# Kernel optimization log

Hardware: AMD Instinct MI355X
Metric: run time of the kernel (lower is better)

Reference implementation:

```python
import jax, jax.numpy as jnp
from jax import lax
import numpy as np


def _conv3x3(x, w, b):
    # x: [B,C,H,W], w: [O,I,3,3] (OIHW), SAME padding, stride 1
    y = lax.conv_general_dilated(x, w, window_strides=(1, 1), padding='SAME',
                                 dimension_numbers=('NCHW', 'OIHW', 'NCHW'))
    return y + b[None, :, None, None]


def setup_inputs() -> dict:
    key = jax.random.key(0)
    ks = jax.random.split(key, 9)
    B, C, H, W = 4, 64, 64, 64
    wscale = 1.0 / np.sqrt(C * 9)  # keep conv outputs / attention logits sane
    x = jax.random.normal(ks[0], (B, C, H, W), dtype=jnp.float32)
    wq = jax.random.normal(ks[1], (C, C, 3, 3), dtype=jnp.float32) * wscale
    bq = jax.random.normal(ks[2], (C,), dtype=jnp.float32) * 0.1
    wk = jax.random.normal(ks[3], (C, C, 3, 3), dtype=jnp.float32) * wscale
    bk = jax.random.normal(ks[4], (C,), dtype=jnp.float32) * 0.1
    wv = jax.random.normal(ks[5], (C, C, 3, 3), dtype=jnp.float32) * wscale
    bv = jax.random.normal(ks[6], (C,), dtype=jnp.float32) * 0.1
    pos_gamma = jax.random.normal(ks[7], (1,), dtype=jnp.float32)
    chan_gamma = jax.random.normal(ks[8], (1,), dtype=jnp.float32)
    return {'x': x, 'wq': wq, 'bq': bq, 'wk': wk, 'bk': bk, 'wv': wv, 'bv': bv,
            'pos_gamma': pos_gamma, 'chan_gamma': chan_gamma}


def reference(x, wq, bq, wk, bk, wv, bv, pos_gamma, chan_gamma):
    B, C, H, W = x.shape
    N = H * W
    # position (spatial) self-attention over N = H*W locations
    q = _conv3x3(x, wq, bq).reshape(B, C, N)
    k = _conv3x3(x, wk, bk).reshape(B, C, N)
    v = _conv3x3(x, wv, bv).reshape(B, C, N)
    # attn[b,i,j] = softmax_j( sum_c q[b,c,i] * k[b,c,j] )
    pos_attn = jax.nn.softmax(jnp.einsum('bci,bcj->bij', q, k), axis=-1)
    # pos_out[b,c,j] = sum_i v[b,c,i] * attn[b,i,j]  (matches torch.bmm(v, attn))
    pos = jnp.einsum('bci,bij->bcj', v, pos_attn).reshape(B, C, H, W)
    pos_out = pos_gamma * pos + x
    # channel self-attention over C channels (x is its own q/k/v)
    xf = x.reshape(B, C, N)
    chan_attn = jax.nn.softmax(jnp.einsum('bcn,bdn->bcd', xf, xf), axis=-1)
    chan = jnp.einsum('bcd,bdn->bcn', chan_attn, xf).reshape(B, C, H, W)
    chan_out = chan_gamma * chan + x
    return pos_out + chan_out
```

## Files before the change

### kernel.cpp

```cpp
#include <hip/hip_runtime.h>

#define OFF_Q2    1048576u
#define OFF_K2    2097152u
#define OFF_V2    3145728u
#define OFF_X2    3670016u
#define OFF_WT    4194304u
#define OFF_INVL  4452352u
#define OFF_A     4730880u
#define WS_FLOATS 4747264u

typedef short s8v __attribute__((ext_vector_type(8)));
typedef float f16v __attribute__((ext_vector_type(16)));

#define MFMA32(a, b, c) __builtin_amdgcn_mfma_f32_32x32x16_bf16((a), (b), (c), 0, 0, 0)

__device__ __forceinline__ unsigned short bf16_rne(float f) {
    union { float f; unsigned int u; } v; v.f = f;
    unsigned int r = v.u + 0x7FFFu + ((v.u >> 16) & 1u);
    return (unsigned short)(r >> 16);
}
__device__ __forceinline__ float bf2f(unsigned short h) {
    union { unsigned int u; float f; } t; t.u = ((unsigned int)h) << 16;
    return t.f;
}
__device__ __forceinline__ void split2(float f, unsigned short& h, unsigned short& l) {
    unsigned short hh = bf16_rne(f);
    h = hh;
    l = bf16_rne(f - bf2f(hh));
}
__device__ __forceinline__ unsigned int cvtpk(float lo, float hi) {
    unsigned int r;
    asm("v_cvt_pk_bf16_f32 %0, %1, %2" : "=v"(r) : "v"(lo), "v"(hi));
    return r;
}
__device__ __forceinline__ void pl32swap(unsigned int& a, unsigned int& b) {
    asm volatile("v_permlane32_swap_b32 %0, %1" : "+v"(a), "+v"(b));
}
__device__ __forceinline__ s8v mk8(unsigned int w0, unsigned int w1,
                                   unsigned int w2, unsigned int w3) {
    union { unsigned int u[4]; s8v v; } t;
    t.u[0] = w0; t.u[1] = w1; t.u[2] = w2; t.u[3] = w3;
    return t.v;
}
__device__ __forceinline__ f16v zero16() {
    f16v z;
#pragma unroll
    for (int i = 0; i < 16; ++i) z[i] = 0.0f;
    return z;
}


__global__ void k_wtrans(const float* __restrict__ wq, const float* __restrict__ wk,
                         const float* __restrict__ wv, unsigned short* __restrict__ wf) {
    int t = blockIdx.x * 256 + threadIdx.x;
    int f = t >> 9, pos = t & 511;
    int lane = pos >> 3, e = pos & 7;
    int oc = f & 1, kst = (f >> 1) & 3;
    int ct = f >> 3;
    int tap = ct % 9, conv = ct / 9;
    int o = oc * 32 + (lane & 31);
    int ci = kst * 16 + (lane >> 5) * 8 + e;
    const float* w = (conv == 0) ? wq : (conv == 1) ? wk : wv;
    float v = w[(o * 64 + ci) * 9 + tap];
    unsigned short hh, ll;
    split2(v, hh, ll);
    wf[(f * 2 + 0) * 512 + pos] = hh;
    wf[(f * 2 + 1) * 512 + pos] = ll;
}

__global__ __launch_bounds__(256) void k_xpack(const float* __restrict__ x,
                                               unsigned short* __restrict__ X2,
                                               unsigned short* __restrict__ XV2) {
    int gid = blockIdx.x * 256 + threadIdx.x;
    int b = gid >> 16;
    int c = (gid >> 10) & 63;
    int n4 = (gid & 1023) * 4;
    float4 v = *(const float4*)(x + (size_t)(b * 64 + c) * 4096 + n4);
    unsigned short hv[4] = {bf16_rne(v.x), bf16_rne(v.y), bf16_rne(v.z), bf16_rne(v.w)};
    int kst = c >> 4, e = c & 7, hb = (c >> 3) & 1;
#pragma unroll
    for (int u = 0; u < 4; ++u) {
        int n = n4 + u;
        int nch = n >> 5, lane = (n & 31) + 32 * hb;
        X2[(size_t)((b * 128 + nch) * 4 + kst) * 512 + lane * 8 + e] = hv[u];
    }
    int ich = n4 >> 5, ksub = (n4 >> 4) & 1, cb = c >> 5;
    int lane2 = (c & 31) + 32 * ((n4 >> 3) & 1);
    size_t xi = (size_t)(((b * 128 + ich) * 2 + ksub) * 2 + cb) * 512 + lane2 * 8 + (n4 & 7);
    unsigned long long w = (unsigned long long)hv[0]
                         | ((unsigned long long)hv[1] << 16)
                         | ((unsigned long long)hv[2] << 32)
                         | ((unsigned long long)hv[3] << 48);
    *(unsigned long long*)(XV2 + xi) = w;
}

__global__ __launch_bounds__(384) void k_conv(
        const float* __restrict__ x, const unsigned short* __restrict__ wf,
        const float* __restrict__ bq, const float* __restrict__ bk, const float* __restrict__ bv,
        unsigned short* __restrict__ Q2, unsigned short* __restrict__ K2,
        unsigned short* __restrict__ V2) {
    int nb = blockIdx.x;
    int b = blockIdx.y;
    int h = nb >> 1, w0 = (nb & 1) * 32;

    __shared__ unsigned short xwh[6528];
    __shared__ unsigned short xwl[6528];

    int tid = threadIdx.x;
    for (int idx = tid; idx < 6528; idx += 384) {
        int W = idx % 34;
        int c = (idx / 34) & 63;
        int dy = idx / (34 * 64);
        int hs = h + dy - 1, wi = w0 + W - 1;
        float v = 0.0f;
        if (hs >= 0 && hs < 64 && wi >= 0 && wi < 64)
            v = x[((b * 64 + c) * 64 + hs) * 64 + wi];
        unsigned short hh_, ll_;
        split2(v, hh_, ll_);
        int row = dy * 34 + W;
        int byt = row * 128 + c * 2;
        int swz = byt ^ ((row & 7) << 4);
        *(unsigned short*)((char*)xwh + swz) = hh_;
        *(unsigned short*)((char*)xwl + swz) = ll_;
    }
    __syncthreads();

    int lane = tid & 63, wv = tid >> 6;
    int conv = wv >> 1, oc = wv & 1;
    int hh = lane >> 5, l31 = lane & 31;

    const float* bias = (conv == 0) ? bq : (conv == 1) ? bk : bv;
    f16v D;
    if (conv < 2) {
#pragma unroll
        for (int r = 0; r < 16; ++r)
            D[r] = bias[oc * 32 + (r & 3) + 8 * (r >> 2) + 4 * hh];
    } else {
        float bvv = bias[oc * 32 + l31];
#pragma unroll
        for (int r = 0; r < 16; ++r) D[r] = bvv;
    }

#pragma unroll
    for (int tap = 0; tap < 9; ++tap) {
        int dy = tap / 3, dx = tap % 3;
#pragma unroll
        for (int kst = 0; kst < 4; ++kst) {
            int f = ((conv * 9 + tap) * 4 + kst) * 2 + oc;
            s8v Wh = *(const s8v*)(wf + (f * 2 + 0) * 512 + lane * 8);
            s8v Wl = *(const s8v*)(wf + (f * 2 + 1) * 512 + lane * 8);
            int row = dy * 34 + dx + l31;
            int byt = row * 128 + kst * 32 + hh * 16;
            int swz = byt ^ ((row & 7) << 4);
            s8v Xh = *(const s8v*)((const char*)xwh + swz);
            s8v Xl = *(const s8v*)((const char*)xwl + swz);
            if (conv < 2) {
                D = MFMA32(Wh, Xh, D);
                D = MFMA32(Wh, Xl, D);
                D = MFMA32(Wl, Xh, D);
            } else {
                D = MFMA32(Xh, Wh, D);
                D = MFMA32(Xl, Wh, D);
                D = MFMA32(Xh, Wl, D);
            }
        }
    }

    if (conv < 2) {
        unsigned short sh[16], sl[16];
#pragma unroll
        for (int r = 0; r < 16; ++r) split2(D[r], sh[r], sl[r]);
        unsigned int ah0 = sh[0] | ((unsigned int)sh[1] << 16), ah1 = sh[2] | ((unsigned int)sh[3] << 16);
        unsigned int ah2 = sh[4] | ((unsigned int)sh[5] << 16), ah3 = sh[6] | ((unsigned int)sh[7] << 16);
        pl32swap(ah0, ah2); pl32swap(ah1, ah3);
        s8v F0h = mk8(ah0, ah1, ah2, ah3);
        unsigned int al0 = sl[0] | ((unsigned int)sl[1] << 16), al1 = sl[2] | ((unsigned int)sl[3] << 16);
        unsigned int al2 = sl[4] | ((unsigned int)sl[5] << 16), al3 = sl[6] | ((unsigned int)sl[7] << 16);
        pl32swap(al0, al2); pl32swap(al1, al3);
        s8v F0l = mk8(al0, al1, al2, al3);
        unsigned int bh0 = sh[8] | ((unsigned int)sh[9] << 16), bh1 = sh[10] | ((unsigned int)sh[11] << 16);
        unsigned int bh2 = sh[12] | ((unsigned int)sh[13] << 16), bh3 = sh[14] | ((unsigned int)sh[15] << 16);
        pl32swap(bh0, bh2); pl32swap(bh1, bh3);
        s8v F1h = mk8(bh0, bh1, bh2, bh3);
        unsigned int bl0 = sl[8] | ((unsigned int)sl[9] << 16), bl1 = sl[10] | ((unsigned int)sl[11] << 16);
        unsigned int bl2 = sl[12] | ((unsigned int)sl[13] << 16), bl3 = sl[14] | ((unsigned int)sl[15] << 16);
        pl32swap(bl0, bl2); pl32swap(bl1, bl3);
        s8v F1l = mk8(bl0, bl1, bl2, bl3);
        unsigned short* dst = (conv == 0) ? Q2 : K2;
        size_t b0 = (size_t)(((b * 128 + nb) * 4 + oc * 2 + 0) * 2) * 512 + lane * 8;
        size_t b1 = (size_t)(((b * 128 + nb) * 4 + oc * 2 + 1) * 2) * 512 + lane * 8;
        *(s8v*)(dst + b0) = F0h;
        *(s8v*)(dst + b0 + 512) = F0l;
        *(s8v*)(dst + b1) = F1h;
        *(s8v*)(dst + b1 + 512) = F1l;
    } else {
        unsigned int a0 = cvtpk(D[0], D[1]),  a1 = cvtpk(D[2], D[3]);
        unsigned int a2 = cvtpk(D[4], D[5]),  a3 = cvtpk(D[6], D[7]);
        pl32swap(a0, a2); pl32swap(a1, a3);
        s8v F0h = mk8(a0, a1, a2, a3);
        unsigned int b0w = cvtpk(D[8], D[9]),  b1w = cvtpk(D[10], D[11]);
        unsigned int b2w = cvtpk(D[12], D[13]), b3w = cvtpk(D[14], D[15]);
        pl32swap(b0w, b2w); pl32swap(b1w, b3w);
        s8v F1h = mk8(b0w, b1w, b2w, b3w);
        size_t v0 = (size_t)(((b * 128 + nb) * 2 + 0) * 2 + oc) * 512 + lane * 8;
        size_t v1 = (size_t)(((b * 128 + nb) * 2 + 1) * 2 + oc) * 512 + lane * 8;
        *(s8v*)(V2 + v0) = F0h;
        *(s8v*)(V2 + v1) = F1h;
    }
}

__global__ __launch_bounds__(256) void k_gram(const unsigned short* __restrict__ XV2,
                                              float* __restrict__ Gp) {
    int kp = blockIdx.x, b = blockIdx.y;
    int tid = threadIdx.x, lane = tid & 63, wv = tid >> 6;
    int cb1 = wv & 1, cb2 = wv >> 1;
    f16v G = zero16();
#pragma unroll 1
    for (int t = 0; t < 32; ++t) {
        int ich = kp * 32 + t;
        const unsigned short* base = XV2 + (size_t)(b * 128 + ich) * 2048 + lane * 8;
        s8v a0 = *(const s8v*)(base + (0 * 2 + cb1) * 512);
        s8v b0 = *(const s8v*)(base + (0 * 2 + cb2) * 512);
        s8v a1 = *(const s8v*)(base + (1 * 2 + cb1) * 512);
        s8v b1 = *(const s8v*)(base + (1 * 2 + cb2) * 512);
        G = MFMA32(a0, b0, G);
        G = MFMA32(a1, b1, G);
    }
    int hh = lane >> 5, l31 = lane & 31;
#pragma unroll
    for (int r = 0; r < 16; ++r) {
        int cc = cb1 * 32 + (r & 3) + 8 * (r >> 2) + 4 * hh;
        int dd = cb2 * 32 + l31;
        Gp[(size_t)(kp * 4 + b) * 4096 + cc * 64 + dd] = G[r];
    }
}

__global__ void k_asm(const float* __restrict__ Gp, unsigned short* __restrict__ A2) {
    int row = blockIdx.x;
    int d = threadIdx.x;
    int b = row >> 6, c = row & 63;
    float g = 0.0f;
#pragma unroll
    for (int p = 0; p < 4; ++p) g += Gp[(size_t)(p * 4 + b) * 4096 + c * 64 + d];
    float mx = g;
    for (int off = 32; off >= 1; off >>= 1) mx = fmaxf(mx, __shfl_xor(mx, off, 64));
    float e = __expf(g - mx);
    float s = e;
    for (int off = 32; off >= 1; off >>= 1) s += __shfl_xor(s, off, 64);
    float a = e / s;
    int cb = c >> 5, kst = d >> 4;
    int lane2 = (c & 31) + 32 * ((d >> 3) & 1);
    A2[(size_t)((b * 2 + cb) * 4 + kst) * 512 + lane2 * 8 + (d & 7)] = bf16_rne(a);
}

__global__ __launch_bounds__(512) void k_pass1(
        const unsigned short* __restrict__ Q2, const unsigned short* __restrict__ K2,
        float* __restrict__ invl) {
    int flat = blockIdx.x;
    int xcd = flat & 7;
    int b = xcd >> 1;
    int ich = (xcd & 1) * 64 + (flat >> 3);
    int tid = threadIdx.x, lane = tid & 63, wv = tid >> 6;

    __shared__ float lsum[8][32];

    const unsigned short* qp = Q2 + (size_t)(b * 128 + ich) * 4096 + lane * 8;
    s8v qf0 = *(const s8v*)(qp);
    s8v qf1 = *(const s8v*)(qp + 512);
    s8v qf2 = *(const s8v*)(qp + 1024);
    s8v qf3 = *(const s8v*)(qp + 1536);
    s8v qf4 = *(const s8v*)(qp + 2048);
    s8v qf5 = *(const s8v*)(qp + 2560);
    s8v qf6 = *(const s8v*)(qp + 3072);
    s8v qf7 = *(const s8v*)(qp + 3584);

    float la0 = 0.f, la1 = 0.f;
#pragma unroll 1
    for (int t = 0; t < 16; ++t) {
        int jch = wv * 16 + t;
        const unsigned short* kp = K2 + (size_t)(b * 128 + jch) * 4096 + lane * 8;
        s8v kf0 = *(const s8v*)(kp);
        s8v kf1 = *(const s8v*)(kp + 512);
        s8v kf2 = *(const s8v*)(kp + 1024);
        s8v kf3 = *(const s8v*)(kp + 1536);
        s8v kf4 = *(const s8v*)(kp + 2048);
        s8v kf5 = *(const s8v*)(kp + 2560);
        s8v kf6 = *(const s8v*)(kp + 3072);
        s8v kf7 = *(const s8v*)(kp + 3584);
        f16v Sa = zero16(), Sb = zero16();
        Sa = MFMA32(kf0, qf0, Sa);
        Sa = MFMA32(kf0, qf1, Sa);
        Sa = MFMA32(kf1, qf0, Sa);
        Sa = MFMA32(kf2, qf2, Sa);
        Sa = MFMA32(kf2, qf3, Sa);
        Sa = MFMA32(kf3, qf2, Sa);
        Sb = MFMA32(kf4, qf4, Sb);
        Sb = MFMA32(kf4, qf5, Sb);
        Sb = MFMA32(kf5, qf4, Sb);
        Sb = MFMA32(kf6, qf6, Sb);
        Sb = MFMA32(kf6, qf7, Sb);
        Sb = MFMA32(kf7, qf6, Sb);
#pragma unroll
        for (int r = 0; r < 8; ++r) la0 += __expf(Sa[r] + Sb[r]);
#pragma unroll
        for (int r = 8; r < 16; ++r) la1 += __expf(Sa[r] + Sb[r]);
    }
    float lacc = la0 + la1;
    lacc += __shfl_xor(lacc, 32);
    if (lane < 32) lsum[wv][lane] = lacc;
    __syncthreads();
    if (tid < 32) {
        float s = 0.f;
#pragma unroll
        for (int p = 0; p < 8; ++p) s += lsum[p][tid];
        invl[b * 4096 + ich * 32 + tid] = 1.0f / s;
    }
}

__global__ __launch_bounds__(256) void k_vnorm(
        unsigned short* __restrict__ V2, const float* __restrict__ invl) {
    int u = blockIdx.x * 256 + threadIdx.x;
    int lane = u & 63, ksub = (u >> 7) & 1;
    int ich = (u >> 8) & 127, b = u >> 15;
    int n0 = ich * 32 + ksub * 16 + (lane >> 5) * 8;
    size_t base = (size_t)u * 8;
    s8v vh = *(s8v*)(V2 + base);
    float4 iv0 = *(const float4*)(invl + b * 4096 + n0);
    float4 iv1 = *(const float4*)(invl + b * 4096 + n0 + 4);
    float ivv[8] = {iv0.x, iv0.y, iv0.z, iv0.w, iv1.x, iv1.y, iv1.z, iv1.w};
    s8v o;
#pragma unroll
    for (int e = 0; e < 8; ++e)
        o[e] = (short)bf16_rne(bf2f((unsigned short)vh[e]) * ivv[e]);
    *(s8v*)(V2 + base) = o;
}

__global__ __launch_bounds__(512) void k_pass2(
        const unsigned short* __restrict__ Q2, const unsigned short* __restrict__ K2,
        const unsigned short* __restrict__ V2, const unsigned short* __restrict__ X2,
        const unsigned short* __restrict__ A2, const float* __restrict__ x,
        const float* __restrict__ pg, const float* __restrict__ cg,
        float* __restrict__ out) {
    int flat = blockIdx.x;
    int xcd = flat & 7;
    int b = xcd >> 1;
    int jt = (xcd & 1) * 64 + (flat >> 3);
    int tid = threadIdx.x, lane = tid & 63, wv = tid >> 6;

    __shared__ float rlds[8][64][32];

    const unsigned short* kp = K2 + (size_t)(b * 128 + jt) * 4096 + lane * 8;
    s8v kf0 = *(const s8v*)(kp);
    s8v kf1 = *(const s8v*)(kp + 512);
    s8v kf2 = *(const s8v*)(kp + 1024);
    s8v kf3 = *(const s8v*)(kp + 1536);
    s8v kf4 = *(const s8v*)(kp + 2048);
    s8v kf5 = *(const s8v*)(kp + 2560);
    s8v kf6 = *(const s8v*)(kp + 3072);
    s8v kf7 = *(const s8v*)(kp + 3584);

    f16v O0 = zero16(), O1 = zero16();

#pragma unroll 1
    for (int t = 0; t < 16; ++t) {
        int ich = wv * 16 + t;
        const unsigned short* qp = Q2 + (size_t)(b * 128 + ich) * 4096 + lane * 8;
        s8v qf0 = *(const s8v*)(qp);
        s8v qf1 = *(const s8v*)(qp + 512);
        s8v qf2 = *(const s8v*)(qp + 1024);
        s8v qf3 = *(const s8v*)(qp + 1536);
        s8v qf4 = *(const s8v*)(qp + 2048);
        s8v qf5 = *(const s8v*)(qp + 2560);
        s8v qf6 = *(const s8v*)(qp + 3072);
        s8v qf7 = *(const s8v*)(qp + 3584);
        const unsigned short* vp = V2 + (size_t)(b * 128 + ich) * 2048 + lane * 8;
        s8v vA = *(const s8v*)(vp);
        s8v vB = *(const s8v*)(vp + 512);
        s8v vC = *(const s8v*)(vp + 1024);
        s8v vD = *(const s8v*)(vp + 1536);

        f16v Sa = zero16(), Sb = zero16();
        Sa = MFMA32(qf0, kf0, Sa);
        Sa = MFMA32(qf0, kf1, Sa);
        Sa = MFMA32(qf1, kf0, Sa);
        Sa = MFMA32(qf2, kf2, Sa);
        Sa = MFMA32(qf2, kf3, Sa);
        Sa = MFMA32(qf3, kf2, Sa);
        Sb = MFMA32(qf4, kf4, Sb);
        Sb = MFMA32(qf4, kf5, Sb);
        Sb = MFMA32(qf5, kf4, Sb);
        Sb = MFMA32(qf6, kf6, Sb);
        Sb = MFMA32(qf6, kf7, Sb);
        Sb = MFMA32(qf7, kf6, Sb);

        float p[16];
#pragma unroll
        for (int r = 0; r < 16; ++r) p[r] = __expf(Sa[r] + Sb[r]);

        unsigned int a0 = cvtpk(p[0], p[1]),  a1 = cvtpk(p[2], p[3]);
        unsigned int a2 = cvtpk(p[4], p[5]),  a3 = cvtpk(p[6], p[7]);
        pl32swap(a0, a2);
        pl32swap(a1, a3);
        s8v P0 = mk8(a0, a1, a2, a3);
        unsigned int b0 = cvtpk(p[8], p[9]),  b1 = cvtpk(p[10], p[11]);
        unsigned int b2 = cvtpk(p[12], p[13]), b3 = cvtpk(p[14], p[15]);
        pl32swap(b0, b2);
        pl32swap(b1, b3);
        s8v P1 = mk8(b0, b1, b2, b3);

        O0 = MFMA32(vA, P0, O0);
        O0 = MFMA32(vC, P1, O0);
        O1 = MFMA32(vB, P0, O1);
        O1 = MFMA32(vD, P1, O1);
    }

    int hh = lane >> 5, jj = lane & 31;
#pragma unroll
    for (int r = 0; r < 16; ++r) {
        int c = (r & 3) + 8 * (r >> 2) + 4 * hh;
        rlds[wv][c][jj] = O0[r];
        rlds[wv][c + 32][jj] = O1[r];
    }
    __syncthreads();
    float sums[4];
#pragma unroll
    for (int k = 0; k < 4; ++k) {
        int el = tid + k * 512;
        int c = el >> 5, j2 = el & 31;
        float s = 0.f;
#pragma unroll
        for (int p = 0; p < 8; ++p) s += rlds[p][c][j2];
        sums[k] = s;
    }
    __syncthreads();
    float* sb = &rlds[0][0][0];
    if (wv < 2) {
        int cb = wv;
        f16v Dc = zero16();
#pragma unroll
        for (int kst = 0; kst < 4; ++kst) {
            s8v af = *(const s8v*)(A2 + (size_t)((b * 2 + cb) * 4 + kst) * 512 + lane * 8);
            s8v xf = *(const s8v*)(X2 + (size_t)((b * 128 + jt) * 4 + kst) * 512 + lane * 8);
            Dc = MFMA32(af, xf, Dc);
        }
#pragma unroll
        for (int r = 0; r < 16; ++r) {
            int c = cb * 32 + (r & 3) + 8 * (r >> 2) + 4 * hh;
            sb[c * 33 + jj] = Dc[r];
        }
    }
#pragma unroll
    for (int k = 0; k < 4; ++k) {
        int el = tid + k * 512;
        int c = el >> 5, j2 = el & 31;
        sb[2112 + el] = x[(size_t)(b * 64 + c) * 4096 + jt * 32 + j2];
    }
    __syncthreads();
    float pgv = pg[0], cgv = cg[0];
#pragma unroll
    for (int k = 0; k < 4; ++k) {
        int el = tid + k * 512;
        int c = el >> 5, j2 = el & 31;
        out[(size_t)(b * 64 + c) * 4096 + jt * 32 + j2] =
            pgv * sums[k] + cgv * sb[c * 33 + j2] + 2.0f * sb[2112 + el];
    }
}

extern "C" void kernel_launch(void* const* d_in, const int* in_sizes, int n_in,
                              void* d_out, int out_size, void* d_ws, size_t ws_size,
                              hipStream_t stream) {
    const float* x  = (const float*)d_in[0];
    const float* wq = (const float*)d_in[1];
    const float* bq = (const float*)d_in[2];
    const float* wk = (const float*)d_in[3];
    const float* bk = (const float*)d_in[4];
    const float* wv = (const float*)d_in[5];
    const float* bv = (const float*)d_in[6];
    const float* pg = (const float*)d_in[7];
    const float* cg = (const float*)d_in[8];
    float* out = (float*)d_out;

    if (ws_size < (size_t)WS_FLOATS * sizeof(float)) return;
    float* ws = (float*)d_ws;
    float* Gp = ws;
    unsigned short* XV2 = (unsigned short*)(ws + 65536);
    unsigned short* Q2  = (unsigned short*)(ws + OFF_Q2);
    unsigned short* K2  = (unsigned short*)(ws + OFF_K2);
    unsigned short* V2  = (unsigned short*)(ws + OFF_V2);
    unsigned short* X2  = (unsigned short*)(ws + OFF_X2);
    unsigned short* wfb = (unsigned short*)(ws + OFF_WT);
    float* invl = ws + OFF_INVL;
    unsigned short* A2  = (unsigned short*)(ws + OFF_A);

    k_wtrans<<<432, 256, 0, stream>>>(wq, wk, wv, wfb);
    k_xpack<<<1024, 256, 0, stream>>>(x, X2, XV2);
    k_conv<<<dim3(128, 4), 384, 0, stream>>>(x, wfb, bq, bk, bv, Q2, K2, V2);
    k_gram<<<dim3(4, 4), 256, 0, stream>>>(XV2, Gp);
    k_asm<<<256, 64, 0, stream>>>(Gp, A2);
    k_pass1<<<512, 512, 0, stream>>>(Q2, K2, invl);
    k_vnorm<<<512, 256, 0, stream>>>(V2, invl);
    k_pass2<<<512, 512, 0, stream>>>(Q2, K2, V2, X2, A2, x, pg, cg, out);
}
```

Measured before the change: 124.8 us.

## Split gram over more blocks, double pass1 waves, halve pass2 reduction LDS

The Gram kernel is split into 16 partial blocks per batch instead of 4, with a fully unrolled 8-step loop, and the assemble kernel sums 16 partials. Gp moves to its own workspace region so the larger partial buffer fits. Pass1 uses 1024-thread blocks with 16 waves, each handling 8 key chunks, for more latency hiding. Pass2 halves its LDS reduction buffer and reduces in two rounds, which may raise occupancy at the cost of extra barriers.

```diff
diff --git a/kernel.cpp b/kernel.cpp
--- a/kernel.cpp
+++ b/kernel.cpp
@@ -1,5 +1,7 @@
 #include <hip/hip_runtime.h>
 
+#define OFF_XV2   65536u
+#define OFF_GP    589824u
 #define OFF_Q2    1048576u
 #define OFF_K2    2097152u
 #define OFF_V2    3145728u
@@ -215,9 +217,9 @@
     int tid = threadIdx.x, lane = tid & 63, wv = tid >> 6;
     int cb1 = wv & 1, cb2 = wv >> 1;
     f16v G = zero16();
-#pragma unroll 1
-    for (int t = 0; t < 32; ++t) {
-        int ich = kp * 32 + t;
+#pragma unroll
+    for (int t = 0; t < 8; ++t) {
+        int ich = kp * 8 + t;
         const unsigned short* base = XV2 + (size_t)(b * 128 + ich) * 2048 + lane * 8;
         s8v a0 = *(const s8v*)(base + (0 * 2 + cb1) * 512);
         s8v b0 = *(const s8v*)(base + (0 * 2 + cb2) * 512);
@@ -241,7 +243,7 @@
     int b = row >> 6, c = row & 63;
     float g = 0.0f;
 #pragma unroll
-    for (int p = 0; p < 4; ++p) g += Gp[(size_t)(p * 4 + b) * 4096 + c * 64 + d];
+    for (int p = 0; p < 16; ++p) g += Gp[(size_t)(p * 4 + b) * 4096 + c * 64 + d];
     float mx = g;
     for (int off = 32; off >= 1; off >>= 1) mx = fmaxf(mx, __shfl_xor(mx, off, 64));
     float e = __expf(g - mx);
@@ -253,7 +255,7 @@
     A2[(size_t)((b * 2 + cb) * 4 + kst) * 512 + lane2 * 8 + (d & 7)] = bf16_rne(a);
 }
 
-__global__ __launch_bounds__(512) void k_pass1(
+__global__ __launch_bounds__(1024) void k_pass1(
         const unsigned short* __restrict__ Q2, const unsigned short* __restrict__ K2,
         float* __restrict__ invl) {
     int flat = blockIdx.x;
@@ -262,7 +264,7 @@
     int ich = (xcd & 1) * 64 + (flat >> 3);
     int tid = threadIdx.x, lane = tid & 63, wv = tid >> 6;
 
-    __shared__ float lsum[8][32];
+    __shared__ float lsum[16][32];
 
     const unsigned short* qp = Q2 + (size_t)(b * 128 + ich) * 4096 + lane * 8;
     s8v qf0 = *(const s8v*)(qp);
@@ -276,8 +278,8 @@
 
     float la0 = 0.f, la1 = 0.f;
 #pragma unroll 1
-    for (int t = 0; t < 16; ++t) {
-        int jch = wv * 16 + t;
+    for (int t = 0; t < 8; ++t) {
+        int jch = wv * 8 + t;
         const unsigned short* kp = K2 + (size_t)(b * 128 + jch) * 4096 + lane * 8;
         s8v kf0 = *(const s8v*)(kp);
         s8v kf1 = *(const s8v*)(kp + 512);
@@ -312,7 +314,7 @@
     if (tid < 32) {
         float s = 0.f;
 #pragma unroll
-        for (int p = 0; p < 8; ++p) s += lsum[p][tid];
+        for (int p = 0; p < 16; ++p) s += lsum[p][tid];
         invl[b * 4096 + ich * 32 + tid] = 1.0f / s;
     }
 }
@@ -347,7 +349,7 @@
     int jt = (xcd & 1) * 64 + (flat >> 3);
     int tid = threadIdx.x, lane = tid & 63, wv = tid >> 6;
 
-    __shared__ float rlds[8][64][32];
+    __shared__ float rlds[4][64][32];
 
     const unsigned short* kp = K2 + (size_t)(b * 128 + jt) * 4096 + lane * 8;
     s8v kf0 = *(const s8v*)(kp);
@@ -415,11 +417,13 @@
     }
 
     int hh = lane >> 5, jj = lane & 31;
-#pragma unroll
-    for (int r = 0; r < 16; ++r) {
-        int c = (r & 3) + 8 * (r >> 2) + 4 * hh;
-        rlds[wv][c][jj] = O0[r];
-        rlds[wv][c + 32][jj] = O1[r];
+    if (wv < 4) {
+#pragma unroll
+        for (int r = 0; r < 16; ++r) {
+            int c = (r & 3) + 8 * (r >> 2) + 4 * hh;
+            rlds[wv][c][jj] = O0[r];
+            rlds[wv][c + 32][jj] = O1[r];
+        }
     }
     __syncthreads();
     float sums[4];
@@ -427,10 +431,24 @@
     for (int k = 0; k < 4; ++k) {
         int el = tid + k * 512;
         int c = el >> 5, j2 = el & 31;
-        float s = 0.f;
-#pragma unroll
-        for (int p = 0; p < 8; ++p) s += rlds[p][c][j2];
-        sums[k] = s;
+        sums[k] = ((rlds[0][c][j2] + rlds[1][c][j2]) + rlds[2][c][j2]) + rlds[3][c][j2];
+    }
+    __syncthreads();
+    if (wv >= 4) {
+#pragma unroll
+        for (int r = 0; r < 16; ++r) {
+            int c = (r & 3) + 8 * (r >> 2) + 4 * hh;
+            rlds[wv - 4][c][jj] = O0[r];
+            rlds[wv - 4][c + 32][jj] = O1[r];
+        }
+    }
+    __syncthreads();
+#pragma unroll
+    for (int k = 0; k < 4; ++k) {
+        int el = tid + k * 512;
+        int c = el >> 5, j2 = el & 31;
+        sums[k] = ((sums[k] + rlds[0][c][j2]) + rlds[1][c][j2]) + rlds[2][c][j2];
+        sums[k] += rlds[3][c][j2];
     }
     __syncthreads();
     float* sb = &rlds[0][0][0];
@@ -482,8 +500,8 @@
 
     if (ws_size < (size_t)WS_FLOATS * sizeof(float)) return;
     float* ws = (float*)d_ws;
-    float* Gp = ws;
-    unsigned short* XV2 = (unsigned short*)(ws + 65536);
+    unsigned short* XV2 = (unsigned short*)(ws + OFF_XV2);
+    float* Gp = ws + OFF_GP;
     unsigned short* Q2  = (unsigned short*)(ws + OFF_Q2);
     unsigned short* K2  = (unsigned short*)(ws + OFF_K2);
     unsigned short* V2  = (unsigned short*)(ws + OFF_V2);
@@ -495,9 +513,9 @@
     k_wtrans<<<432, 256, 0, stream>>>(wq, wk, wv, wfb);
     k_xpack<<<1024, 256, 0, stream>>>(x, X2, XV2);
     k_conv<<<dim3(128, 4), 384, 0, stream>>>(x, wfb, bq, bk, bv, Q2, K2, V2);
-    k_gram<<<dim3(4, 4), 256, 0, stream>>>(XV2, Gp);
+    k_gram<<<dim3(16, 4), 256, 0, stream>>>(XV2, Gp);
     k_asm<<<256, 64, 0, stream>>>(Gp, A2);
-    k_pass1<<<512, 512, 0, stream>>>(Q2, K2, invl);
+    k_pass1<<<512, 1024, 0, stream>>>(Q2, K2, invl);
     k_vnorm<<<512, 256, 0, stream>>>(V2, invl);
     k_pass2<<<512, 512, 0, stream>>>(Q2, K2, V2, X2, A2, x, pg, cg, out);
 }
```

Measured after the change: 120.0 us. 3.9% less time.
